# Performance work log

Measured on AMD Instinct MI355X. Metric: run time of the kernel, lower is better.

Reference implementation:

```python
import jax, jax.numpy as jnp
import numpy as np

N, E = 16384, 8192
IN_FT, OUT_FT = 256, 128


def setup_inputs() -> dict:
    key = jax.random.key(0)
    k1, k2, k3, k4, k5 = jax.random.split(key, 5)
    stdv = 1.0 / np.sqrt(OUT_FT)
    return {
        "x": jax.random.normal(k1, (N, IN_FT), dtype=jnp.float32),
        "weight": jax.random.uniform(k2, (IN_FT, OUT_FT), dtype=jnp.float32, minval=-stdv, maxval=stdv),
        "MT": jax.random.uniform(k3, (E, N), dtype=jnp.float32),  # hyperedge incidence [E, N]
        "D_v_diag": jax.random.uniform(k4, (E,), dtype=jnp.float32),  # diagonal of edge-degree matrix [E, E]
        "D_e_diag": jax.random.uniform(k5, (N,), dtype=jnp.float32),  # diagonal of node-degree matrix [N, N]
    }


def reference(x, weight, MT, D_v_diag, D_e_diag):
    # linear projection (bias=None in original)
    y = x @ weight                                   # [N, OUT_FT]
    # 0.5 * D_e @ MT.T @ D_v @ MT @ y, with diagonal degree matrices as row scalings
    ey = MT @ y                                      # [E, OUT_FT] node->edge aggregation
    ey = D_v_diag[:, None] * ey                      # edge-degree scaling
    ny = MT.T @ ey                                   # [N, OUT_FT] edge->node aggregation
    return 0.5 * D_e_diag[:, None] * ny
```

## Files before the change

### kernel.cpp

```cpp
#include <hip/hip_runtime.h>

#define NN 16384
#define EE 8192
#define KIN 256
#define FOUT 128

typedef short short8 __attribute__((ext_vector_type(8)));
typedef short short4v __attribute__((ext_vector_type(4)));
typedef float f32x4 __attribute__((ext_vector_type(4)));
typedef __bf16 bf16x8 __attribute__((ext_vector_type(8)));

__device__ inline unsigned short f2bf(float f) {
    union { float f; unsigned u; } v; v.f = f;
    unsigned r = v.u + 0x7fffu + ((v.u >> 16) & 1u);
    return (unsigned short)(r >> 16);
}

__device__ inline f32x4 mfma_bf16(short8 a, short8 b, f32x4 c) {
    union { short8 s; bf16x8 h; } ua, ub;
    ua.s = a; ub.s = b;
    return __builtin_amdgcn_mfma_f32_16x16x32_bf16(ua.h, ub.h, c, 0, 0, 0);
}

__global__ __launch_bounds__(256) void k1_xw_yT(
    const float* __restrict__ x, const float* __restrict__ w,
    unsigned short* __restrict__ yT) {
    __shared__ union {
        unsigned short wT[FOUT * KIN];
        unsigned short cT[FOUT * 72];
    } sm;
    const int t  = threadIdx.x;
    const int l  = t & 63;
    const int wv = t >> 6;
    const int q4 = l >> 4;

    {
        const int f  = t >> 1;
        const int kh = (t & 1) * 128;
        #pragma unroll 4
        for (int q = 0; q < 16; ++q) {
            short8 pk;
            #pragma unroll
            for (int j = 0; j < 8; ++j)
                pk[j] = (short)f2bf(w[(kh + q * 8 + j) * FOUT + f]);
            int c = ((kh >> 3) + q) ^ (f & 7);
            *(short8*)&sm.wT[f * KIN + c * 8] = pk;
        }
    }
    __syncthreads();

    const int nBase = blockIdx.x * 64;
    const int n = nBase + wv * 16 + (l & 15);
    f32x4 acc[8];
    #pragma unroll
    for (int i = 0; i < 8; ++i) acc[i] = (f32x4)0.0f;

    #pragma unroll
    for (int kk = 0; kk < 8; ++kk) {
        const float* xr = x + (size_t)n * KIN + kk * 32 + q4 * 8;
        float4 v0 = *(const float4*)xr;
        float4 v1 = *(const float4*)(xr + 4);
        short8 a;
        a[0] = (short)f2bf(v0.x); a[1] = (short)f2bf(v0.y);
        a[2] = (short)f2bf(v0.z); a[3] = (short)f2bf(v0.w);
        a[4] = (short)f2bf(v1.x); a[5] = (short)f2bf(v1.y);
        a[6] = (short)f2bf(v1.z); a[7] = (short)f2bf(v1.w);
        #pragma unroll
        for (int ft = 0; ft < 8; ++ft) {
            int f = ft * 16 + (l & 15);
            int c = (kk * 4 + q4) ^ (f & 7);
            short8 b = *(const short8*)&sm.wT[f * KIN + c * 8];
            acc[ft] = mfma_bf16(a, b, acc[ft]);
        }
    }
    __syncthreads();

    #pragma unroll
    for (int ft = 0; ft < 8; ++ft) {
        short4v pk;
        #pragma unroll
        for (int r = 0; r < 4; ++r) pk[r] = (short)f2bf(acc[ft][r]);
        int f = ft * 16 + (l & 15);
        *(short4v*)&sm.cT[f * 72 + wv * 16 + q4 * 4] = pk;
    }
    __syncthreads();
    {
        const int f  = t >> 1;
        const int nh = (t & 1) * 32;
        #pragma unroll
        for (int qq = 0; qq < 4; ++qq) {
            short8 v = *(const short8*)&sm.cT[f * 72 + nh + qq * 8];
            *(short8*)&yT[(size_t)f * NN + nBase + nh + qq * 8] = v;
        }
    }
}

__global__ __launch_bounds__(256) void k2_mt_y(
    const float* __restrict__ MT, const unsigned short* __restrict__ yT,
    const float* __restrict__ dv, float* __restrict__ eyf) {
    __shared__ unsigned short blds[FOUT * 64];
    const int t  = threadIdx.x;
    const int l  = t & 63;
    const int wv = t >> 6;
    const int q4 = l >> 4;
    const int eBase = blockIdx.x * 64;
    const int s = blockIdx.y;
    const int e = eBase + wv * 16 + (l & 15);
    const float sA = dv[e];
    const float* arow = MT + (size_t)e * NN;

    f32x4 acc[8];
    #pragma unroll
    for (int i = 0; i < 8; ++i) acc[i] = (f32x4)0.0f;

    const int sf = t >> 1;
    const int skoff = (t & 1) * 32;
    const int scb = skoff >> 3;
    const int sfx = sf & 7;

    for (int cc = 0; cc < 64; ++cc) {
        const int k0 = s * 4096 + cc * 64;
        {
            const unsigned short* src = yT + (size_t)sf * NN + k0 + skoff;
            short8 v0 = *(const short8*)(src);
            short8 v1 = *(const short8*)(src + 8);
            short8 v2 = *(const short8*)(src + 16);
            short8 v3 = *(const short8*)(src + 24);
            *(short8*)&blds[sf * 64 + ((scb + 0) ^ sfx) * 8] = v0;
            *(short8*)&blds[sf * 64 + ((scb + 1) ^ sfx) * 8] = v1;
            *(short8*)&blds[sf * 64 + ((scb + 2) ^ sfx) * 8] = v2;
            *(short8*)&blds[sf * 64 + ((scb + 3) ^ sfx) * 8] = v3;
        }
        __syncthreads();
        #pragma unroll
        for (int kk = 0; kk < 2; ++kk) {
            const float* ar = arow + k0 + kk * 32 + q4 * 8;
            float4 v0 = *(const float4*)ar;
            float4 v1 = *(const float4*)(ar + 4);
            short8 a;
            a[0] = (short)f2bf(sA * v0.x); a[1] = (short)f2bf(sA * v0.y);
            a[2] = (short)f2bf(sA * v0.z); a[3] = (short)f2bf(sA * v0.w);
            a[4] = (short)f2bf(sA * v1.x); a[5] = (short)f2bf(sA * v1.y);
            a[6] = (short)f2bf(sA * v1.z); a[7] = (short)f2bf(sA * v1.w);
            #pragma unroll
            for (int ft = 0; ft < 8; ++ft) {
                int f = ft * 16 + (l & 15);
                int c = (kk * 4 + q4) ^ (f & 7);
                short8 b = *(const short8*)&blds[f * 64 + c * 8];
                acc[ft] = mfma_bf16(a, b, acc[ft]);
            }
        }
        __syncthreads();
    }
    #pragma unroll
    for (int ft = 0; ft < 8; ++ft) {
        int f  = ft * 16 + (l & 15);
        int eo = eBase + wv * 16 + q4 * 4;
        #pragma unroll
        for (int r = 0; r < 4; ++r)
            atomicAdd(&eyf[(size_t)(eo + r) * FOUT + f], acc[ft][r]);
    }
}

__global__ __launch_bounds__(256) void k2b_cvtT(
    const float* __restrict__ eyf, unsigned short* __restrict__ eyT) {
    int idx = blockIdx.x * 256 + threadIdx.x;
    int e8 = idx & 1023;
    int f  = idx >> 10;
    short8 pk;
    #pragma unroll
    for (int j = 0; j < 8; ++j)
        pk[j] = (short)f2bf(eyf[(size_t)(e8 * 8 + j) * FOUT + f]);
    *(short8*)&eyT[(size_t)f * EE + e8 * 8] = pk;
}

__global__ __launch_bounds__(256) void k3_mtT_ey(
    const float* __restrict__ MT, const unsigned short* __restrict__ eyT,
    const float* __restrict__ de, float* __restrict__ out) {
    __shared__ unsigned short blds[FOUT * 64];
    const int t  = threadIdx.x;
    const int l  = t & 63;
    const int wv = t >> 6;
    const int q4 = l >> 4;
    const int nBase = blockIdx.x * 64;
    const int s = blockIdx.y;
    const int n = nBase + wv * 16 + (l & 15);
    const float sA = 0.5f * de[n];

    f32x4 acc[8];
    #pragma unroll
    for (int i = 0; i < 8; ++i) acc[i] = (f32x4)0.0f;

    const int sf = t >> 1;
    const int skoff = (t & 1) * 32;
    const int scb = skoff >> 3;
    const int sfx = sf & 7;

    for (int cc = 0; cc < 64; ++cc) {
        const int k0 = s * 4096 + cc * 64;
        {
            const unsigned short* src = eyT + (size_t)sf * EE + k0 + skoff;
            short8 v0 = *(const short8*)(src);
            short8 v1 = *(const short8*)(src + 8);
            short8 v2 = *(const short8*)(src + 16);
            short8 v3 = *(const short8*)(src + 24);
            *(short8*)&blds[sf * 64 + ((scb + 0) ^ sfx) * 8] = v0;
            *(short8*)&blds[sf * 64 + ((scb + 1) ^ sfx) * 8] = v1;
            *(short8*)&blds[sf * 64 + ((scb + 2) ^ sfx) * 8] = v2;
            *(short8*)&blds[sf * 64 + ((scb + 3) ^ sfx) * 8] = v3;
        }
        __syncthreads();
        #pragma unroll
        for (int kk = 0; kk < 2; ++kk) {
            const float* ap = MT + (size_t)(k0 + kk * 32 + q4 * 8) * NN + n;
            float av[8];
            #pragma unroll
            for (int j = 0; j < 8; ++j) av[j] = ap[(size_t)j * NN];
            short8 a;
            #pragma unroll
            for (int j = 0; j < 8; ++j) a[j] = (short)f2bf(sA * av[j]);
            #pragma unroll
            for (int ft = 0; ft < 8; ++ft) {
                int f = ft * 16 + (l & 15);
                int c = (kk * 4 + q4) ^ (f & 7);
                short8 b = *(const short8*)&blds[f * 64 + c * 8];
                acc[ft] = mfma_bf16(a, b, acc[ft]);
            }
        }
        __syncthreads();
    }
    #pragma unroll
    for (int ft = 0; ft < 8; ++ft) {
        int f  = ft * 16 + (l & 15);
        int no = nBase + wv * 16 + q4 * 4;
        #pragma unroll
        for (int r = 0; r < 4; ++r)
            atomicAdd(&out[(size_t)(no + r) * FOUT + f], acc[ft][r]);
    }
}

extern "C" void kernel_launch(void* const* d_in, const int* in_sizes, int n_in,
                              void* d_out, int out_size, void* d_ws, size_t ws_size,
                              hipStream_t stream) {
    const float* x  = (const float*)d_in[0];
    const float* w  = (const float*)d_in[1];
    const float* MT = (const float*)d_in[2];
    const float* dv = (const float*)d_in[3];
    const float* de = (const float*)d_in[4];
    float* out = (float*)d_out;

    char* ws = (char*)d_ws;
    unsigned short* yT  = (unsigned short*)(ws);
    unsigned short* eyT = (unsigned short*)(ws + (4u << 20));
    float*          eyf = (float*)(ws + (6u << 20));

    hipMemsetAsync(out, 0, (size_t)NN * FOUT * sizeof(float), stream);
    hipMemsetAsync(eyf, 0, (size_t)EE * FOUT * sizeof(float), stream);

    k1_xw_yT <<<256, 256, 0, stream>>>(x, w, yT);
    k2_mt_y  <<<dim3(128, 4), 256, 0, stream>>>(MT, yT, dv, eyf);
    k2b_cvtT <<<512, 256, 0, stream>>>(eyf, eyT);
    k3_mtT_ey<<<dim3(256, 2), 256, 0, stream>>>(MT, eyT, de, out);
}
```

Baseline: 977.2 us.

## Double-buffer LDS tiles and double split-K grid in both MT GEMM kernels

Both MT-streaming kernels now double-buffer the shared-memory B tile. The next tile is prefetched into registers while the MFMAs run on the current buffer, which removes one barrier per iteration. The split-K factor is doubled (grid y 4→8 and 2→4) so more blocks are in flight, and launch bounds request 4 blocks per CU. In exchange there are twice as many float atomics on the outputs, and the LDS footprint doubles.

```diff
diff --git a/kernel.cpp b/kernel.cpp
--- a/kernel.cpp
+++ b/kernel.cpp
@@ -95,16 +95,16 @@
     }
 }
 
-__global__ __launch_bounds__(256) void k2_mt_y(
+__global__ __launch_bounds__(256, 4) void k2_mt_y(
     const float* __restrict__ MT, const unsigned short* __restrict__ yT,
     const float* __restrict__ dv, float* __restrict__ eyf) {
-    __shared__ unsigned short blds[FOUT * 64];
+    __shared__ unsigned short blds[2][FOUT * 64];
     const int t  = threadIdx.x;
     const int l  = t & 63;
     const int wv = t >> 6;
     const int q4 = l >> 4;
     const int eBase = blockIdx.x * 64;
-    const int s = blockIdx.y;
+    const int sBase = blockIdx.y * 2048;
     const int e = eBase + wv * 16 + (l & 15);
     const float sA = dv[e];
     const float* arow = MT + (size_t)e * NN;
@@ -117,40 +117,61 @@
     const int skoff = (t & 1) * 32;
     const int scb = skoff >> 3;
     const int sfx = sf & 7;
-
-    for (int cc = 0; cc < 64; ++cc) {
-        const int k0 = s * 4096 + cc * 64;
-        {
-            const unsigned short* src = yT + (size_t)sf * NN + k0 + skoff;
-            short8 v0 = *(const short8*)(src);
-            short8 v1 = *(const short8*)(src + 8);
-            short8 v2 = *(const short8*)(src + 16);
-            short8 v3 = *(const short8*)(src + 24);
-            *(short8*)&blds[sf * 64 + ((scb + 0) ^ sfx) * 8] = v0;
-            *(short8*)&blds[sf * 64 + ((scb + 1) ^ sfx) * 8] = v1;
-            *(short8*)&blds[sf * 64 + ((scb + 2) ^ sfx) * 8] = v2;
-            *(short8*)&blds[sf * 64 + ((scb + 3) ^ sfx) * 8] = v3;
-        }
+    const unsigned short* srcBase = yT + (size_t)sf * NN + skoff;
+
+    {
+        const unsigned short* src = srcBase + sBase;
+        short8 v0 = *(const short8*)(src);
+        short8 v1 = *(const short8*)(src + 8);
+        short8 v2 = *(const short8*)(src + 16);
+        short8 v3 = *(const short8*)(src + 24);
+        *(short8*)&blds[0][sf * 64 + ((scb + 0) ^ sfx) * 8] = v0;
+        *(short8*)&blds[0][sf * 64 + ((scb + 1) ^ sfx) * 8] = v1;
+        *(short8*)&blds[0][sf * 64 + ((scb + 2) ^ sfx) * 8] = v2;
+        *(short8*)&blds[0][sf * 64 + ((scb + 3) ^ sfx) * 8] = v3;
+    }
+
+    for (int cc = 0; cc < 32; ++cc) {
+        const int k0 = sBase + cc * 64;
         __syncthreads();
+
+        float4 a0[2], a1[2];
         #pragma unroll
         for (int kk = 0; kk < 2; ++kk) {
             const float* ar = arow + k0 + kk * 32 + q4 * 8;
-            float4 v0 = *(const float4*)ar;
-            float4 v1 = *(const float4*)(ar + 4);
+            a0[kk] = *(const float4*)ar;
+            a1[kk] = *(const float4*)(ar + 4);
+        }
+        short8 v0, v1, v2, v3;
+        if (cc != 31) {
+            const unsigned short* src = srcBase + k0 + 64;
+            v0 = *(const short8*)(src);
+            v1 = *(const short8*)(src + 8);
+            v2 = *(const short8*)(src + 16);
+            v3 = *(const short8*)(src + 24);
+        }
+        #pragma unroll
+        for (int kk = 0; kk < 2; ++kk) {
             short8 a;
-            a[0] = (short)f2bf(sA * v0.x); a[1] = (short)f2bf(sA * v0.y);
-            a[2] = (short)f2bf(sA * v0.z); a[3] = (short)f2bf(sA * v0.w);
-            a[4] = (short)f2bf(sA * v1.x); a[5] = (short)f2bf(sA * v1.y);
-            a[6] = (short)f2bf(sA * v1.z); a[7] = (short)f2bf(sA * v1.w);
+            a[0] = (short)f2bf(sA * a0[kk].x); a[1] = (short)f2bf(sA * a0[kk].y);
+            a[2] = (short)f2bf(sA * a0[kk].z); a[3] = (short)f2bf(sA * a0[kk].w);
+            a[4] = (short)f2bf(sA * a1[kk].x); a[5] = (short)f2bf(sA * a1[kk].y);
+            a[6] = (short)f2bf(sA * a1[kk].z); a[7] = (short)f2bf(sA * a1[kk].w);
             #pragma unroll
             for (int ft = 0; ft < 8; ++ft) {
                 int f = ft * 16 + (l & 15);
                 int c = (kk * 4 + q4) ^ (f & 7);
-                short8 b = *(const short8*)&blds[f * 64 + c * 8];
+                short8 b = *(const short8*)&blds[cc & 1][f * 64 + c * 8];
                 acc[ft] = mfma_bf16(a, b, acc[ft]);
             }
         }
-        __syncthreads();
+        if (cc != 31) {
+            unsigned short* dst = &blds[(cc + 1) & 1][sf * 64];
+            *(short8*)&dst[((scb + 0) ^ sfx) * 8] = v0;
+            *(short8*)&dst[((scb + 1) ^ sfx) * 8] = v1;
+            *(short8*)&dst[((scb + 2) ^ sfx) * 8] = v2;
+            *(short8*)&dst[((scb + 3) ^ sfx) * 8] = v3;
+        }
     }
     #pragma unroll
     for (int ft = 0; ft < 8; ++ft) {
@@ -174,16 +195,16 @@
     *(short8*)&eyT[(size_t)f * EE + e8 * 8] = pk;
 }
 
-__global__ __launch_bounds__(256) void k3_mtT_ey(
+__global__ __launch_bounds__(256, 4) void k3_mtT_ey(
     const float* __restrict__ MT, const unsigned short* __restrict__ eyT,
     const float* __restrict__ de, float* __restrict__ out) {
-    __shared__ unsigned short blds[FOUT * 64];
+    __shared__ unsigned short blds[2][FOUT * 64];
     const int t  = threadIdx.x;
     const int l  = t & 63;
     const int wv = t >> 6;
     const int q4 = l >> 4;
     const int nBase = blockIdx.x * 64;
-    const int s = blockIdx.y;
+    const int sBase = blockIdx.y * 2048;
     const int n = nBase + wv * 16 + (l & 15);
     const float sA = 0.5f * de[n];
 
@@ -195,39 +216,59 @@
     const int skoff = (t & 1) * 32;
     const int scb = skoff >> 3;
     const int sfx = sf & 7;
-
-    for (int cc = 0; cc < 64; ++cc) {
-        const int k0 = s * 4096 + cc * 64;
-        {
-            const unsigned short* src = eyT + (size_t)sf * EE + k0 + skoff;
-            short8 v0 = *(const short8*)(src);
-            short8 v1 = *(const short8*)(src + 8);
-            short8 v2 = *(const short8*)(src + 16);
-            short8 v3 = *(const short8*)(src + 24);
-            *(short8*)&blds[sf * 64 + ((scb + 0) ^ sfx) * 8] = v0;
-            *(short8*)&blds[sf * 64 + ((scb + 1) ^ sfx) * 8] = v1;
-            *(short8*)&blds[sf * 64 + ((scb + 2) ^ sfx) * 8] = v2;
-            *(short8*)&blds[sf * 64 + ((scb + 3) ^ sfx) * 8] = v3;
-        }
+    const unsigned short* srcBase = eyT + (size_t)sf * EE + skoff;
+
+    {
+        const unsigned short* src = srcBase + sBase;
+        short8 v0 = *(const short8*)(src);
+        short8 v1 = *(const short8*)(src + 8);
+        short8 v2 = *(const short8*)(src + 16);
+        short8 v3 = *(const short8*)(src + 24);
+        *(short8*)&blds[0][sf * 64 + ((scb + 0) ^ sfx) * 8] = v0;
+        *(short8*)&blds[0][sf * 64 + ((scb + 1) ^ sfx) * 8] = v1;
+        *(short8*)&blds[0][sf * 64 + ((scb + 2) ^ sfx) * 8] = v2;
+        *(short8*)&blds[0][sf * 64 + ((scb + 3) ^ sfx) * 8] = v3;
+    }
+
+    for (int cc = 0; cc < 32; ++cc) {
+        const int k0 = sBase + cc * 64;
         __syncthreads();
+
+        float av[2][8];
         #pragma unroll
         for (int kk = 0; kk < 2; ++kk) {
             const float* ap = MT + (size_t)(k0 + kk * 32 + q4 * 8) * NN + n;
-            float av[8];
-            #pragma unroll
-            for (int j = 0; j < 8; ++j) av[j] = ap[(size_t)j * NN];
+            #pragma unroll
+            for (int j = 0; j < 8; ++j) av[kk][j] = ap[(size_t)j * NN];
+        }
+        short8 v0, v1, v2, v3;
+        if (cc != 31) {
+            const unsigned short* src = srcBase + k0 + 64;
+            v0 = *(const short8*)(src);
+            v1 = *(const short8*)(src + 8);
+            v2 = *(const short8*)(src + 16);
+            v3 = *(const short8*)(src + 24);
+        }
+        #pragma unroll
+        for (int kk = 0; kk < 2; ++kk) {
             short8 a;
             #pragma unroll
-            for (int j = 0; j < 8; ++j) a[j] = (short)f2bf(sA * av[j]);
+            for (int j = 0; j < 8; ++j) a[j] = (short)f2bf(sA * av[kk][j]);
             #pragma unroll
             for (int ft = 0; ft < 8; ++ft) {
                 int f = ft * 16 + (l & 15);
                 int c = (kk * 4 + q4) ^ (f & 7);
-                short8 b = *(const short8*)&blds[f * 64 + c * 8];
+                short8 b = *(const short8*)&blds[cc & 1][f * 64 + c * 8];
                 acc[ft] = mfma_bf16(a, b, acc[ft]);
             }
         }
-        __syncthreads();
+        if (cc != 31) {
+            unsigned short* dst = &blds[(cc + 1) & 1][sf * 64];
+            *(short8*)&dst[((scb + 0) ^ sfx) * 8] = v0;
+            *(short8*)&dst[((scb + 1) ^ sfx) * 8] = v1;
+            *(short8*)&dst[((scb + 2) ^ sfx) * 8] = v2;
+            *(short8*)&dst[((scb + 3) ^ sfx) * 8] = v3;
+        }
     }
     #pragma unroll
     for (int ft = 0; ft < 8; ++ft) {
@@ -258,7 +299,7 @@
     hipMemsetAsync(eyf, 0, (size_t)EE * FOUT * sizeof(float), stream);
 
     k1_xw_yT <<<256, 256, 0, stream>>>(x, w, yT);
-    k2_mt_y  <<<dim3(128, 4), 256, 0, stream>>>(MT, yT, dv, eyf);
+    k2_mt_y  <<<dim3(128, 8), 256, 0, stream>>>(MT, yT, dv, eyf);
     k2b_cvtT <<<512, 256, 0, stream>>>(eyf, eyT);
-    k3_mtT_ey<<<dim3(256, 2), 256, 0, stream>>>(MT, eyT, de, out);
-}
+    k3_mtT_ey<<<dim3(256, 4), 256, 0, stream>>>(MT, eyT, de, out);
+}
```

After: 906.6 us. 1.08x faster.
